# Kernel optimization log

Hardware: AMD Instinct MI355X
Metric: run time of the kernel (lower is better)

Reference implementation:

```python
import jax, jax.numpy as jnp
import numpy as np

B, D, N = 2048, 512, 100000


def setup_inputs() -> dict:
    key = jax.random.key(0)
    k1, k2, k3 = jax.random.split(key, 3)
    queries = jax.random.normal(k1, (B, D), dtype=jnp.float32)
    X = jax.random.normal(k2, (N, D), dtype=jnp.float32)
    Y = jax.random.randint(k3, (N,), 0, 2, dtype=jnp.int64)
    return {"queries": queries, "X": X, "Y": Y, "K": 5}


def reference(queries, X, Y, K):
    # Pairwise squared Euclidean distance: ||q||^2 - 2 q.X^T + ||x||^2.
    # Use negative distance so lax.top_k returns nearest neighbors.
    q2 = jnp.sum(queries * queries, axis=1, keepdims=True)        # [B, 1]
    x2 = jnp.sum(X * X, axis=1)                                   # [N]
    neg_dist = 2.0 * (queries @ X.T) - q2 - x2[None, :]           # [B, N]
    _, idx = jax.lax.top_k(neg_dist, K)                           # [B, K]
    # Gather neighbor labels and count votes (fraction of class-1 neighbors).
    neighbor_labels = Y[idx].astype(jnp.float32)                  # [B, K]
    votes = jnp.mean(neighbor_labels, axis=1)                     # [B]
    # tf.pad(tf.expand_dims(votes, 1), [[0,0],[0,1]]) -> [B, 2]
    return jnp.pad(votes[:, None], ((0, 0), (0, 1)))
```

## Files before the change

### kernel.cpp

```cpp
#include <hip/hip_runtime.h>
#include <math.h>

typedef unsigned int   u32;
typedef unsigned short u16;
typedef short short8 __attribute__((ext_vector_type(8)));
typedef float f32x4   __attribute__((ext_vector_type(4)));
typedef float f32x16  __attribute__((ext_vector_type(16)));

constexpr int B    = 2048;
constexpr int D    = 512;
constexpr int N    = 100000;
constexpr int KTOP = 5;
constexpr int NK   = 16;

constexpr int NPART    = 48;
constexpr int CHUNK    = 2112;
constexpr int ITERS    = CHUNK / 32;
constexpr int NPTS_PAD = NPART * CHUNK;
constexpr int NPG32    = NPTS_PAD / 32;

__device__ __forceinline__ u16 f2bf(float f) {
    u32 u = __float_as_uint(f);
    return (u16)((u + 0x7fffu + ((u >> 16) & 1u)) >> 16);
}

__device__ __forceinline__ void gld_lds16(const void* g, void* l) {
    __builtin_amdgcn_global_load_lds((const __attribute__((address_space(1))) u32*)g,
                                     (__attribute__((address_space(3))) u32*)l, 16, 0, 0);
}

__device__ __forceinline__ void ins5(float (&s)[KTOP], int (&x)[KTOP], float v, int p) {
    if (v > s[KTOP - 1]) {
        s[KTOP - 1] = v; x[KTOP - 1] = p;
#pragma unroll
        for (int k = KTOP - 1; k > 0; --k) {
            if (s[k] > s[k - 1]) {
                float tf = s[k]; s[k] = s[k - 1]; s[k - 1] = tf;
                int   tg = x[k]; x[k] = x[k - 1]; x[k - 1] = tg;
            }
        }
    }
}

__device__ __forceinline__ void merge_xor(float (&s)[KTOP], int (&x)[KTOP], int mask) {
    float bs[KTOP], as[KTOP]; int bx[KTOP], ax[KTOP];
#pragma unroll
    for (int k = 0; k < KTOP; ++k) {
        bs[k] = __shfl_xor(s[k], mask); bx[k] = __shfl_xor(x[k], mask);
        as[k] = s[k]; ax[k] = x[k];
    }
#pragma unroll
    for (int k = 0; k < KTOP; ++k) {
        bool ta = (as[0] > bs[0]) || ((as[0] == bs[0]) && (ax[0] < bx[0]));
        s[k] = ta ? as[0] : bs[0];
        x[k] = ta ? ax[0] : bx[0];
#pragma unroll
        for (int m = 0; m < KTOP - 1; ++m) {
            as[m] = ta ? as[m + 1] : as[m];     ax[m] = ta ? ax[m + 1] : ax[m];
            bs[m] = ta ? bs[m]     : bs[m + 1]; bx[m] = ta ? bx[m]     : bx[m + 1];
        }
        as[KTOP - 1] = ta ? -INFINITY : as[KTOP - 1];
        bs[KTOP - 1] = ta ? bs[KTOP - 1] : -INFINITY;
    }
}

__global__ void prep_q32(const float* __restrict__ Q, u16* __restrict__ Qbf) {
    int tid  = blockIdx.x * 256 + threadIdx.x;
    int q    = tid >> 6;
    int koct = tid & 63;
    const float4* src = (const float4*)(Q + (size_t)q * D + koct * 8);
    float4 a = src[0], b = src[1];
    u32 p0 = (u32)f2bf(a.x) | ((u32)f2bf(a.y) << 16);
    u32 p1 = (u32)f2bf(a.z) | ((u32)f2bf(a.w) << 16);
    u32 p2 = (u32)f2bf(b.x) | ((u32)f2bf(b.y) << 16);
    u32 p3 = (u32)f2bf(b.z) | ((u32)f2bf(b.w) << 16);
    int kstep = koct >> 1, octet = koct & 1;
    int lane  = (q & 31) + 32 * octet;
    size_t frag = (size_t)(q >> 5) * 32 + kstep;
    *(uint4*)(Qbf + (frag * 64 + lane) * 8) = make_uint4(p0, p1, p2, p3);
}

__global__ void prep_q16(const float* __restrict__ Q, u16* __restrict__ Qbf) {
    int tid  = blockIdx.x * 256 + threadIdx.x;
    int q    = tid >> 6;
    int koct = tid & 63;
    const float4* src = (const float4*)(Q + (size_t)q * D + koct * 8);
    float4 a = src[0], b = src[1];
    u32 p0 = (u32)f2bf(a.x) | ((u32)f2bf(a.y) << 16);
    u32 p1 = (u32)f2bf(a.z) | ((u32)f2bf(a.w) << 16);
    u32 p2 = (u32)f2bf(b.x) | ((u32)f2bf(b.y) << 16);
    u32 p3 = (u32)f2bf(b.z) | ((u32)f2bf(b.w) << 16);
    int frag = (q >> 4) * NK + (koct >> 2);
    int lane = (q & 15) + 16 * (koct & 3);
    *(uint4*)(Qbf + (size_t)frag * 512 + lane * 8) = make_uint4(p0, p1, p2, p3);
}

__global__ void prep_x2(const float* __restrict__ X, u16* __restrict__ Xbf,
                        float* __restrict__ x2) {
    __shared__ __attribute__((aligned(16))) u16 Xl[32][520];
    const int t = threadIdx.x, lane = t & 63, wave = t >> 6;
    const int pg = blockIdx.x;
#pragma unroll
    for (int i = 0; i < 8; ++i) {
        const int p     = wave * 8 + i;
        const int point = pg * 32 + p;
        float4 a = make_float4(0.f, 0.f, 0.f, 0.f), b = a;
        if (point < N) {
            const float4* src = (const float4*)(X + (size_t)point * D + lane * 8);
            a = src[0]; b = src[1];
        }
        float s = 0.f;
        s = fmaf(a.x, a.x, s); s = fmaf(a.y, a.y, s);
        s = fmaf(a.z, a.z, s); s = fmaf(a.w, a.w, s);
        s = fmaf(b.x, b.x, s); s = fmaf(b.y, b.y, s);
        s = fmaf(b.z, b.z, s); s = fmaf(b.w, b.w, s);
        u32 p0 = (u32)f2bf(a.x) | ((u32)f2bf(a.y) << 16);
        u32 p1 = (u32)f2bf(a.z) | ((u32)f2bf(a.w) << 16);
        u32 p2 = (u32)f2bf(b.x) | ((u32)f2bf(b.y) << 16);
        u32 p3 = (u32)f2bf(b.z) | ((u32)f2bf(b.w) << 16);
        *(uint4*)&Xl[p][lane * 8] = make_uint4(p0, p1, p2, p3);
        s += __shfl_xor(s, 1);  s += __shfl_xor(s, 2);  s += __shfl_xor(s, 4);
        s += __shfl_xor(s, 8);  s += __shfl_xor(s, 16); s += __shfl_xor(s, 32);
        if (lane == 0) x2[pg * 32 + p] = (point < N) ? s : INFINITY;
    }
    __syncthreads();
#pragma unroll
    for (int v = 0; v < 8; ++v) {
        const int ks = v * 4 + wave;
        uint4 o = *(const uint4*)&Xl[lane & 31][ks * 16 + (lane >> 5) * 8];
        *(uint4*)(Xbf + (((size_t)pg * 32 + ks) * 64 + lane) * 8) = o;
    }
}

__global__ void x2_kernel(const float* __restrict__ X, float* __restrict__ x2, int total) {
    int lane = threadIdx.x & 63;
    int wid  = (int)((blockIdx.x * blockDim.x + threadIdx.x) >> 6);
    if (wid >= total) return;
    if (wid >= N) { if (lane == 0) x2[wid] = INFINITY; return; }
    const float* row = X + (size_t)wid * D;
    float s = 0.f;
    for (int c = lane; c < D; c += 64) { float v = row[c]; s = fmaf(v, v, s); }
#pragma unroll
    for (int off = 32; off > 0; off >>= 1) s += __shfl_down(s, off);
    if (lane == 0) x2[wid] = s;
}

__launch_bounds__(256, 3)
__global__ void knn_qreg(const u16* __restrict__ Xbf, const u16* __restrict__ Qbf,
                         const float* __restrict__ x2g,
                         float* __restrict__ cand_s, int* __restrict__ cand_i) {
    __shared__ __attribute__((aligned(16))) u16 Afr[4][8 * 512];
    __shared__ __attribute__((aligned(16))) float x2s[CHUNK];
    const int t    = threadIdx.x;
    const int lane = t & 63;
    const int wave = t >> 6;
    const int hid  = lane >> 5;
    const int col  = lane & 31;
    const int part = blockIdx.x;
    const int qb   = blockIdx.y;
    const int pg0    = part * ITERS;
    const int pstart = part * CHUNK;

    const int qg = qb * 4 + wave;
    short8 bq[32];
#pragma unroll
    for (int ks = 0; ks < 32; ++ks)
        bq[ks] = *(const short8*)(Qbf + (((size_t)qg * 32 + ks) * 64 + lane) * 8);
    asm volatile("" ::: "memory");

    for (int i = t; i < CHUNK / 4; i += 256)
        ((float4*)x2s)[i] = ((const float4*)(x2g + pstart))[i];

    float ss[KTOP]; int si[KTOP];
#pragma unroll
    for (int k = 0; k < KTOP; ++k) { ss[k] = -INFINITY; si[k] = 0x7fffffff; }

    auto issue = [&](int ph) {
        const int buf = ph & 3;
        const size_t fb = ((size_t)(pg0 + (ph >> 2)) * 32 + (ph & 3) * 8 + wave * 2) * 64;
        const u16* src = Xbf + (fb + lane) * 8;
        u16* dst = &Afr[buf][(wave * 2) * 512 + lane * 8];
        gld_lds16(src, dst);
        gld_lds16(src + 512, dst + 512);
    };

    auto epi = [&](const f32x16& acc, int it) {
        const int base = it * 32 + hid * 4;
        float4 xx0 = *(const float4*)&x2s[base];
        float4 xx1 = *(const float4*)&x2s[base + 8];
        float4 xx2 = *(const float4*)&x2s[base + 16];
        float4 xx3 = *(const float4*)&x2s[base + 24];
        const int PA = pstart + base;
        float s0  = fmaf(2.f, acc[0],  -xx0.x), s1  = fmaf(2.f, acc[1],  -xx0.y);
        float s2  = fmaf(2.f, acc[2],  -xx0.z), s3  = fmaf(2.f, acc[3],  -xx0.w);
        float s4  = fmaf(2.f, acc[4],  -xx1.x), s5  = fmaf(2.f, acc[5],  -xx1.y);
        float s6  = fmaf(2.f, acc[6],  -xx1.z), s7  = fmaf(2.f, acc[7],  -xx1.w);
        float s8  = fmaf(2.f, acc[8],  -xx2.x), s9  = fmaf(2.f, acc[9],  -xx2.y);
        float s10 = fmaf(2.f, acc[10], -xx2.z), s11 = fmaf(2.f, acc[11], -xx2.w);
        float s12 = fmaf(2.f, acc[12], -xx3.x), s13 = fmaf(2.f, acc[13], -xx3.y);
        float s14 = fmaf(2.f, acc[14], -xx3.z), s15 = fmaf(2.f, acc[15], -xx3.w);
        float m0 = fmaxf(fmaxf(s0, s1),   fmaxf(s2, s3));
        float m1 = fmaxf(fmaxf(s4, s5),   fmaxf(s6, s7));
        float m2 = fmaxf(fmaxf(s8, s9),   fmaxf(s10, s11));
        float m3 = fmaxf(fmaxf(s12, s13), fmaxf(s14, s15));
        float mx = fmaxf(fmaxf(m0, m1), fmaxf(m2, m3));
        if (mx > ss[KTOP - 1]) {
            ins5(ss, si, s0,  PA + 0);  ins5(ss, si, s1,  PA + 1);
            ins5(ss, si, s2,  PA + 2);  ins5(ss, si, s3,  PA + 3);
            ins5(ss, si, s4,  PA + 8);  ins5(ss, si, s5,  PA + 9);
            ins5(ss, si, s6,  PA + 10); ins5(ss, si, s7,  PA + 11);
            ins5(ss, si, s8,  PA + 16); ins5(ss, si, s9,  PA + 17);
            ins5(ss, si, s10, PA + 18); ins5(ss, si, s11, PA + 19);
            ins5(ss, si, s12, PA + 24); ins5(ss, si, s13, PA + 25);
            ins5(ss, si, s14, PA + 26); ins5(ss, si, s15, PA + 27);
        }
    };

#define WBAR(NSTR) asm volatile("s_waitcnt vmcnt(" NSTR ")\n\ts_barrier" ::: "memory")

    __syncthreads();
    issue(0); issue(1); issue(2);

    for (int it = 0; it < ITERS - 1; ++it) {
        f32x16 acc = (f32x16)0.f;
#pragma unroll
        for (int sub = 0; sub < 4; ++sub) {
            WBAR("4");
            issue(it * 4 + sub + 3);
#pragma unroll
            for (int k = 0; k < 8; ++k) {
                short8 af = *(const short8*)&Afr[sub][k * 512 + lane * 8];
                acc = __builtin_amdgcn_mfma_f32_32x32x16_bf16(af, bq[sub * 8 + k], acc, 0, 0, 0);
            }
        }
        epi(acc, it);
    }
    {
        const int it = ITERS - 1;
        f32x16 acc = (f32x16)0.f;
        WBAR("4");
        issue(it * 4 + 3);
#pragma unroll
        for (int k = 0; k < 8; ++k) {
            short8 af = *(const short8*)&Afr[0][k * 512 + lane * 8];
            acc = __builtin_amdgcn_mfma_f32_32x32x16_bf16(af, bq[k], acc, 0, 0, 0);
        }
        WBAR("4");
#pragma unroll
        for (int k = 0; k < 8; ++k) {
            short8 af = *(const short8*)&Afr[1][k * 512 + lane * 8];
            acc = __builtin_amdgcn_mfma_f32_32x32x16_bf16(af, bq[8 + k], acc, 0, 0, 0);
        }
        WBAR("2");
#pragma unroll
        for (int k = 0; k < 8; ++k) {
            short8 af = *(const short8*)&Afr[2][k * 512 + lane * 8];
            acc = __builtin_amdgcn_mfma_f32_32x32x16_bf16(af, bq[16 + k], acc, 0, 0, 0);
        }
        WBAR("0");
#pragma unroll
        for (int k = 0; k < 8; ++k) {
            short8 af = *(const short8*)&Afr[3][k * 512 + lane * 8];
            acc = __builtin_amdgcn_mfma_f32_32x32x16_bf16(af, bq[24 + k], acc, 0, 0, 0);
        }
        epi(acc, it);
    }
#undef WBAR

    merge_xor(ss, si, 32);
    if (hid == 0) {
        int q = qg * 32 + col;
        size_t base = ((size_t)q * NPART + part) * KTOP;
#pragma unroll
        for (int k = 0; k < KTOP; ++k) { cand_s[base + k] = ss[k]; cand_i[base + k] = si[k]; }
    }
}

__launch_bounds__(256)
__global__ void knn_conv(const float* __restrict__ X, const u16* __restrict__ Qbf,
                         const float* __restrict__ x2g,
                         float* __restrict__ cand_s, int* __restrict__ cand_i) {
    __shared__ __attribute__((aligned(16))) u16 Bfr[16 * 512];
    __shared__ __attribute__((aligned(16))) u16 Afr[4 * 512];
    __shared__ float x2s[64];
    const int t = threadIdx.x, lane = t & 63, wave = t >> 6;
    const int quad = lane >> 4, col = lane & 15;
    const int qb = blockIdx.x, part = blockIdx.y;
    const int pstart = part * 782;
    const int pend   = min(pstart + 782, N);

    float ss[4][KTOP]; int si[4][KTOP];
#pragma unroll
    for (int j = 0; j < 4; ++j)
#pragma unroll
        for (int k = 0; k < KTOP; ++k) { ss[j][k] = -INFINITY; si[j][k] = 0x7fffffff; }

    const int nsub = (pend - pstart + 63) / 64;
    for (int sbi = 0; sbi < nsub; ++sbi) {
        const int sb = pstart + sbi * 64;
        __syncthreads();
        if (t < 64) x2s[t] = (sb + t < pend) ? x2g[sb + t] : INFINITY;
        f32x4 acc[4][4];
#pragma unroll
        for (int i = 0; i < 4; ++i)
#pragma unroll
            for (int j = 0; j < 4; ++j) acc[i][j] = (f32x4)0.f;
        for (int k0i = 0; k0i < NK; ++k0i) {
            const int k0 = k0i * 32;
            __syncthreads();
            {
                int prow = sb + wave * 16 + col;
                if (prow >= pend) prow = pend - 1;
                const float4* src = (const float4*)(X + (size_t)prow * D + k0 + quad * 8);
                float4 a = src[0], b = src[1];
                u32 p0 = (u32)f2bf(a.x) | ((u32)f2bf(a.y) << 16);
                u32 p1 = (u32)f2bf(a.z) | ((u32)f2bf(a.w) << 16);
                u32 p2 = (u32)f2bf(b.x) | ((u32)f2bf(b.y) << 16);
                u32 p3 = (u32)f2bf(b.z) | ((u32)f2bf(b.w) << 16);
                *(uint4*)(Afr + wave * 512 + lane * 8) = make_uint4(p0, p1, p2, p3);
            }
#pragma unroll
            for (int j = 0; j < 4; ++j) {
                int qgrp = qb * 16 + wave * 4 + j;
                gld_lds16(Qbf + ((size_t)qgrp * NK + k0i) * 512 + lane * 8,
                          (void*)(Bfr + (wave * 4 + j) * 512));
            }
            __syncthreads();
            short8 af[4], bqf[4];
#pragma unroll
            for (int i = 0; i < 4; ++i) af[i] = *(const short8*)(Afr + i * 512 + lane * 8);
#pragma unroll
            for (int j = 0; j < 4; ++j) bqf[j] = *(const short8*)(Bfr + (wave * 4 + j) * 512 + lane * 8);
#pragma unroll
            for (int i = 0; i < 4; ++i)
#pragma unroll
                for (int j = 0; j < 4; ++j)
                    acc[i][j] = __builtin_amdgcn_mfma_f32_16x16x32_bf16(af[i], bqf[j], acc[i][j], 0, 0, 0);
        }
#pragma unroll
        for (int i = 0; i < 4; ++i) {
            int pb = 16 * i + quad * 4;
#pragma unroll
            for (int j = 0; j < 4; ++j)
#pragma unroll
                for (int r = 0; r < 4; ++r)
                    ins5(ss[j], si[j], 2.f * acc[i][j][r] - x2s[pb + r], sb + pb + r);
        }
    }
#pragma unroll
    for (int j = 0; j < 4; ++j) { merge_xor(ss[j], si[j], 16); merge_xor(ss[j], si[j], 32); }
    if (quad == 0) {
#pragma unroll
        for (int j = 0; j < 4; ++j) {
            int qg = qb * 256 + wave * 64 + j * 16 + col;
            size_t base = ((size_t)qg * 128 + part) * KTOP;
#pragma unroll
            for (int k = 0; k < KTOP; ++k) { cand_s[base + k] = ss[j][k]; cand_i[base + k] = si[j][k]; }
        }
    }
}

__launch_bounds__(256)
__global__ void finalize(const float* __restrict__ Q, const float* __restrict__ X,
                         const float* __restrict__ x2g, const int* __restrict__ Y,
                         const float* __restrict__ cand_s, const int* __restrict__ cand_i,
                         float* __restrict__ out, int npart) {
    __shared__ float scs[4][96];
    __shared__ int   sis[4][96];
    const int t = threadIdx.x, lane = t & 63, w = t >> 6;
    const int q = blockIdx.x * 4 + w;
    const int perlane = npart * KTOP / 16;

    if (lane < 16) {
        float ls[KTOP]; int li[KTOP];
#pragma unroll
        for (int k = 0; k < KTOP; ++k) { ls[k] = -INFINITY; li[k] = 0x7fffffff; }
        const float* cs = cand_s + (size_t)q * npart * KTOP + lane * perlane;
        const int*   ci = cand_i + (size_t)q * npart * KTOP + lane * perlane;
        for (int c = 0; c < perlane; ++c) {
            float s = cs[c]; int p = ci[c];
            if (s > ls[KTOP - 1] || (s == ls[KTOP - 1] && p < li[KTOP - 1])) {
                ls[KTOP - 1] = s; li[KTOP - 1] = p;
#pragma unroll
                for (int k = KTOP - 1; k > 0; --k) {
                    bool up = (ls[k] > ls[k - 1]) || (ls[k] == ls[k - 1] && li[k] < li[k - 1]);
                    if (up) {
                        float tf = ls[k]; ls[k] = ls[k - 1]; ls[k - 1] = tf;
                        int   tg = li[k]; li[k] = li[k - 1]; li[k - 1] = tg;
                    }
                }
            }
        }
#pragma unroll
        for (int k = 0; k < KTOP; ++k) { scs[w][lane * KTOP + k] = ls[k]; sis[w][lane * KTOP + k] = li[k]; }
    }
    __syncthreads();
    if (lane == 0) {
        float bs[16]; int bx[16];
#pragma unroll
        for (int m = 0; m < 16; ++m) { bs[m] = -INFINITY; bx[m] = 0x7fffffff; }
        for (int c = 0; c < 80; ++c) {
            float s = scs[w][c]; int p = sis[w][c];
            if (s > bs[15] || (s == bs[15] && p < bx[15])) {
                bs[15] = s; bx[15] = p;
#pragma unroll
                for (int m = 15; m > 0; --m) {
                    bool up = (bs[m] > bs[m - 1]) || (bs[m] == bs[m - 1] && bx[m] < bx[m - 1]);
                    if (up) {
                        float tf = bs[m]; bs[m] = bs[m - 1]; bs[m - 1] = tf;
                        int   tg = bx[m]; bx[m] = bx[m - 1]; bx[m - 1] = tg;
                    }
                }
            }
        }
#pragma unroll
        for (int m = 0; m < 16; ++m) sis[w][80 + m] = bx[m];
    }
    __syncthreads();
    const int c = lane & 15, seg = lane >> 4;
    int idx = sis[w][80 + c];
    const float4* xr = (const float4*)(X + (size_t)idx * D);
    const float4* qr = (const float4*)(Q + (size_t)q * D);
    float d = 0.f;
    for (int u = seg * 32; u < seg * 32 + 32; ++u) {
        float4 a = qr[u], b = xr[u];
        d = fmaf(a.x, b.x, d); d = fmaf(a.y, b.y, d);
        d = fmaf(a.z, b.z, d); d = fmaf(a.w, b.w, d);
    }
    d += __shfl_xor(d, 16);
    d += __shfl_xor(d, 32);
    float sc = 2.f * d - x2g[idx];
    if (seg == 0) scs[w][80 + c] = sc;
    __syncthreads();
    if (lane == 0) {
        float bs[KTOP]; int bx[KTOP];
#pragma unroll
        for (int k = 0; k < KTOP; ++k) { bs[k] = -INFINITY; bx[k] = 0x7fffffff; }
        for (int c2 = 0; c2 < 16; ++c2) {
            float s = scs[w][80 + c2]; int p = sis[w][80 + c2];
            if (s > bs[KTOP - 1] || (s == bs[KTOP - 1] && p < bx[KTOP - 1])) {
                bs[KTOP - 1] = s; bx[KTOP - 1] = p;
#pragma unroll
                for (int k = KTOP - 1; k > 0; --k) {
                    bool up = (bs[k] > bs[k - 1]) || (bs[k] == bs[k - 1] && bx[k] < bx[k - 1]);
                    if (up) {
                        float tf = bs[k]; bs[k] = bs[k - 1]; bs[k - 1] = tf;
                        int   tg = bx[k]; bx[k] = bx[k - 1]; bx[k - 1] = tg;
                    }
                }
            }
        }
        float sum = 0.f;
#pragma unroll
        for (int k = 0; k < KTOP; ++k) sum += (float)Y[bx[k]];
        out[2 * q]     = sum * 0.2f;
        out[2 * q + 1] = 0.f;
    }
}

extern "C" void kernel_launch(void* const* d_in, const int* in_sizes, int n_in,
                              void* d_out, int out_size, void* d_ws, size_t ws_size,
                              hipStream_t stream) {
    const float* Qf = (const float*)d_in[0];
    const float* Xf = (const float*)d_in[1];
    const int*   Y  = (const int*)d_in[2];
    float* out = (float*)d_out;
    char* ws = (char*)d_ws;

    constexpr size_t XBF_B  = (size_t)NPTS_PAD * D * 2;
    constexpr size_t QBF_B  = 2097152;
    constexpr size_t X2_B   = (size_t)NPTS_PAD * 4;
    constexpr size_t CAND_B = (size_t)B * NPART * KTOP * 4;
    constexpr size_t NEED   = XBF_B + QBF_B + X2_B + 2 * CAND_B;

    if (ws_size >= NEED) {
        u16*   Xbf    = (u16*)ws;
        u16*   Qbf    = (u16*)(ws + XBF_B);
        float* x2     = (float*)(ws + XBF_B + QBF_B);
        float* cand_s = (float*)(ws + XBF_B + QBF_B + X2_B);
        int*   cand_i = (int*)  (ws + XBF_B + QBF_B + X2_B + CAND_B);
        hipLaunchKernelGGL(prep_q32, dim3(512),       dim3(256), 0, stream, Qf, Qbf);
        hipLaunchKernelGGL(prep_x2,  dim3(NPG32),     dim3(256), 0, stream, Xf, Xbf, x2);
        hipLaunchKernelGGL(knn_qreg, dim3(NPART, 16), dim3(256), 0, stream, Xbf, Qbf, x2, cand_s, cand_i);
        hipLaunchKernelGGL(finalize, dim3(B / 4),     dim3(256), 0, stream, Qf, Xf, x2, Y, cand_s, cand_i, out, NPART);
    } else {
        u16*   Qbf    = (u16*)ws;
        float* x2     = (float*)(ws + 2097152);
        float* cand_s = (float*)(ws + 2497152);
        int*   cand_i = (int*)  (ws + 7740032);
        hipLaunchKernelGGL(prep_q16,  dim3(512),      dim3(256), 0, stream, Qf, Qbf);
        hipLaunchKernelGGL(x2_kernel, dim3(N / 4),    dim3(256), 0, stream, Xf, x2, N);
        hipLaunchKernelGGL(knn_conv,  dim3(8, 128),   dim3(256), 0, stream, Xf, Qbf, x2, cand_s, cand_i);
        hipLaunchKernelGGL(finalize,  dim3(B / 4),    dim3(256), 0, stream, Qf, Xf, x2, Y, cand_s, cand_i, out, 128);
    }
}
```

Measured before the change: 655.2 us.

## Use 8-wave blocks sharing X tiles with a 6-deep LDS pipeline

The knn_qreg blocks grow from 4 to 8 waves (8 query groups), so each X tile staged in LDS feeds twice as many queries. Each wave now issues a single 16-byte global-to-LDS load per phase, and the pipeline ring deepens to 6 buffers with 5 phases in flight. The partition grid changes from 48 chunks of 2112 points to 64 chunks of 1568, which changes padding, grid shape and how many candidates finalize has to merge. Possible costs are lower occupancy from the 512-thread launch bounds and slower barriers across 8 waves.

```diff
diff --git a/kernel.cpp b/kernel.cpp
--- a/kernel.cpp
+++ b/kernel.cpp
@@ -13,11 +13,12 @@
 constexpr int KTOP = 5;
 constexpr int NK   = 16;
 
-constexpr int NPART    = 48;
-constexpr int CHUNK    = 2112;
+constexpr int NPART    = 64;
+constexpr int CHUNK    = 1568;
 constexpr int ITERS    = CHUNK / 32;
 constexpr int NPTS_PAD = NPART * CHUNK;
 constexpr int NPG32    = NPTS_PAD / 32;
+constexpr int NPH      = ITERS * 4;
 
 __device__ __forceinline__ u16 f2bf(float f) {
     u32 u = __float_as_uint(f);
@@ -145,11 +146,11 @@
     if (lane == 0) x2[wid] = s;
 }
 
-__launch_bounds__(256, 3)
+__launch_bounds__(512, 2)
 __global__ void knn_qreg(const u16* __restrict__ Xbf, const u16* __restrict__ Qbf,
                          const float* __restrict__ x2g,
                          float* __restrict__ cand_s, int* __restrict__ cand_i) {
-    __shared__ __attribute__((aligned(16))) u16 Afr[4][8 * 512];
+    __shared__ __attribute__((aligned(16))) u16 Afr[6][8 * 512];
     __shared__ __attribute__((aligned(16))) float x2s[CHUNK];
     const int t    = threadIdx.x;
     const int lane = t & 63;
@@ -161,27 +162,25 @@
     const int pg0    = part * ITERS;
     const int pstart = part * CHUNK;
 
-    const int qg = qb * 4 + wave;
+    const int qg = qb * 8 + wave;
     short8 bq[32];
 #pragma unroll
     for (int ks = 0; ks < 32; ++ks)
         bq[ks] = *(const short8*)(Qbf + (((size_t)qg * 32 + ks) * 64 + lane) * 8);
     asm volatile("" ::: "memory");
 
-    for (int i = t; i < CHUNK / 4; i += 256)
+    for (int i = t; i < CHUNK / 4; i += 512)
         ((float4*)x2s)[i] = ((const float4*)(x2g + pstart))[i];
 
     float ss[KTOP]; int si[KTOP];
 #pragma unroll
     for (int k = 0; k < KTOP; ++k) { ss[k] = -INFINITY; si[k] = 0x7fffffff; }
 
-    auto issue = [&](int ph) {
-        const int buf = ph & 3;
-        const size_t fb = ((size_t)(pg0 + (ph >> 2)) * 32 + (ph & 3) * 8 + wave * 2) * 64;
-        const u16* src = Xbf + (fb + lane) * 8;
-        u16* dst = &Afr[buf][(wave * 2) * 512 + lane * 8];
-        gld_lds16(src, dst);
-        gld_lds16(src + 512, dst + 512);
+    const u16* srcNext = Xbf + (((size_t)pg0 * 32 + wave) * 64 + lane) * 8;
+    u16* const d0 = &Afr[0][wave * 512 + lane * 8];
+    auto issueN = [&](int buf) {
+        gld_lds16(srcNext, d0 + buf * 4096);
+        srcNext += 4096;
     };
 
     auto epi = [&](const f32x16& acc, int it) {
@@ -216,56 +215,55 @@
         }
     };
 
-#define WBAR(NSTR) asm volatile("s_waitcnt vmcnt(" NSTR ")\n\ts_barrier" ::: "memory")
+#define WB(NSTR) asm volatile("s_waitcnt vmcnt(" NSTR ")\n\ts_barrier" ::: "memory")
 
     __syncthreads();
-    issue(0); issue(1); issue(2);
-
-    for (int it = 0; it < ITERS - 1; ++it) {
-        f32x16 acc = (f32x16)0.f;
-#pragma unroll
-        for (int sub = 0; sub < 4; ++sub) {
-            WBAR("4");
-            issue(it * 4 + sub + 3);
+    issueN(0); issueN(1); issueN(2); issueN(3); issueN(4);
+
+    f32x16 acc = (f32x16)0.f;
+    for (int m = 0; m < 16; ++m) {
+#pragma unroll
+        for (int j = 0; j < 12; ++j) {
+            WB("4");
+            if (j < 11 || m < 15) issueN((j + 5) % 6);
+            if ((j & 3) == 0) acc = (f32x16)0.f;
 #pragma unroll
             for (int k = 0; k < 8; ++k) {
-                short8 af = *(const short8*)&Afr[sub][k * 512 + lane * 8];
-                acc = __builtin_amdgcn_mfma_f32_32x32x16_bf16(af, bq[sub * 8 + k], acc, 0, 0, 0);
-            }
-        }
-        epi(acc, it);
+                short8 af = *(const short8*)&Afr[j % 6][k * 512 + lane * 8];
+                acc = __builtin_amdgcn_mfma_f32_32x32x16_bf16(af, bq[(j & 3) * 8 + k], acc, 0, 0, 0);
+            }
+            if ((j & 3) == 3) epi(acc, 3 * m + (j >> 2));
+        }
     }
     {
-        const int it = ITERS - 1;
-        f32x16 acc = (f32x16)0.f;
-        WBAR("4");
-        issue(it * 4 + 3);
+        acc = (f32x16)0.f;
+        WB("3");
 #pragma unroll
         for (int k = 0; k < 8; ++k) {
             short8 af = *(const short8*)&Afr[0][k * 512 + lane * 8];
             acc = __builtin_amdgcn_mfma_f32_32x32x16_bf16(af, bq[k], acc, 0, 0, 0);
         }
-        WBAR("4");
+        WB("2");
 #pragma unroll
         for (int k = 0; k < 8; ++k) {
             short8 af = *(const short8*)&Afr[1][k * 512 + lane * 8];
             acc = __builtin_amdgcn_mfma_f32_32x32x16_bf16(af, bq[8 + k], acc, 0, 0, 0);
         }
-        WBAR("2");
+        WB("1");
 #pragma unroll
         for (int k = 0; k < 8; ++k) {
             short8 af = *(const short8*)&Afr[2][k * 512 + lane * 8];
             acc = __builtin_amdgcn_mfma_f32_32x32x16_bf16(af, bq[16 + k], acc, 0, 0, 0);
         }
-        WBAR("0");
+        WB("0");
 #pragma unroll
         for (int k = 0; k < 8; ++k) {
             short8 af = *(const short8*)&Afr[3][k * 512 + lane * 8];
             acc = __builtin_amdgcn_mfma_f32_32x32x16_bf16(af, bq[24 + k], acc, 0, 0, 0);
         }
-        epi(acc, it);
-    }
-#undef WBAR
+        epi(acc, ITERS - 1);
+    }
+#undef WB
 
     merge_xor(ss, si, 32);
     if (hid == 0) {
@@ -479,18 +477,18 @@
         float* x2     = (float*)(ws + XBF_B + QBF_B);
         float* cand_s = (float*)(ws + XBF_B + QBF_B + X2_B);
         int*   cand_i = (int*)  (ws + XBF_B + QBF_B + X2_B + CAND_B);
-        hipLaunchKernelGGL(prep_q32, dim3(512),       dim3(256), 0, stream, Qf, Qbf);
-        hipLaunchKernelGGL(prep_x2,  dim3(NPG32),     dim3(256), 0, stream, Xf, Xbf, x2);
-        hipLaunchKernelGGL(knn_qreg, dim3(NPART, 16), dim3(256), 0, stream, Xbf, Qbf, x2, cand_s, cand_i);
-        hipLaunchKernelGGL(finalize, dim3(B / 4),     dim3(256), 0, stream, Qf, Xf, x2, Y, cand_s, cand_i, out, NPART);
+        hipLaunchKernelGGL(prep_q32, dim3(512),      dim3(256), 0, stream, Qf, Qbf);
+        hipLaunchKernelGGL(prep_x2,  dim3(NPG32),    dim3(256), 0, stream, Xf, Xbf, x2);
+        hipLaunchKernelGGL(knn_qreg, dim3(NPART, 8), dim3(512), 0, stream, Xbf, Qbf, x2, cand_s, cand_i);
+        hipLaunchKernelGGL(finalize, dim3(B / 4),    dim3(256), 0, stream, Qf, Xf, x2, Y, cand_s, cand_i, out, NPART);
     } else {
         u16*   Qbf    = (u16*)ws;
         float* x2     = (float*)(ws + 2097152);
         float* cand_s = (float*)(ws + 2497152);
         int*   cand_i = (int*)  (ws + 7740032);
-        hipLaunchKernelGGL(prep_q16,  dim3(512),      dim3(256), 0, stream, Qf, Qbf);
-        hipLaunchKernelGGL(x2_kernel, dim3(N / 4),    dim3(256), 0, stream, Xf, x2, N);
-        hipLaunchKernelGGL(knn_conv,  dim3(8, 128),   dim3(256), 0, stream, Xf, Qbf, x2, cand_s, cand_i);
-        hipLaunchKernelGGL(finalize,  dim3(B / 4),    dim3(256), 0, stream, Qf, Xf, x2, Y, cand_s, cand_i, out, 128);
-    }
-}
+        hipLaunchKernelGGL(prep_q16,  dim3(512),     dim3(256), 0, stream, Qf, Qbf);
+        hipLaunchKernelGGL(x2_kernel, dim3(N / 4),   dim3(256), 0, stream, Xf, x2, N);
+        hipLaunchKernelGGL(knn_conv,  dim3(8, 128),  dim3(256), 0, stream, Xf, Qbf, x2, cand_s, cand_i);
+        hipLaunchKernelGGL(finalize,  dim3(B / 4),   dim3(256), 0, stream, Qf, Xf, x2, Y, cand_s, cand_i, out, 128);
+    }
+}
```

Result: slower. 676.8 us (+3.3%).
